# Performance work log

Measured on AMD Instinct MI355X. Metric: run time of the kernel, lower is better.

## Reference

```python
import jax, jax.numpy as jnp
import numpy as np

B, D, T, H, K = 16, 1024, 1024, 1024, 2  # batch, in_channels, seq_len, hidden_size, kernel_size


def setup_inputs() -> dict:
    key = jax.random.key(0)
    k1, k2, k3 = jax.random.split(key, 3)
    inputs = jax.random.normal(k1, (B, D, T), dtype=jnp.float32)
    # Conv1D kernel in OIH layout: [3H, D, K]; scaled to keep gates in a sane range
    conv_w = jax.random.normal(k2, (3 * H, D, K), dtype=jnp.float32) / np.float32(np.sqrt(D * K))
    conv_b = jax.random.normal(k3, (3 * H,), dtype=jnp.float32) * 0.01
    return {"inputs": inputs, "conv_w": conv_w, "conv_b": conv_b}


def reference(inputs, conv_w, conv_b):
    # inputs: [B, D, T] (channels_first, as in the keras call signature)
    # Causal conv: left-pad time by K-1, then VALID conv -> [B, 3H, T]
    padded = jnp.pad(inputs, ((0, 0), (0, 0), (K - 1, 0)))
    gates = jax.lax.conv_general_dilated(
        padded, conv_w, window_strides=(1,), padding="VALID",
        dimension_numbers=("NCH", "OIH", "NCH"))
    gates = gates + conv_b[None, :, None]
    gates = jnp.transpose(gates, (0, 2, 1))  # [B, T, 3H]
    z = jnp.tanh(gates[..., :H])
    f = jax.nn.sigmoid(gates[..., H:2 * H])
    o = jax.nn.sigmoid(gates[..., 2 * H:])

    # fo-pooling linear recurrence: c_t = f_t * c_{t-1} + (1 - f_t) * z_t, c_0 = 0
    zf = (jnp.transpose(z, (1, 0, 2)), jnp.transpose(f, (1, 0, 2)))  # time-major [T, B, H]

    def step(c, zf_t):
        z_t, f_t = zf_t
        c_new = f_t * c + (1.0 - f_t) * z_t
        return c_new, c_new

    c0 = jnp.zeros((B, H), dtype=inputs.dtype)
    _, c_seq = jax.lax.scan(step, c0, zf)
    c_seq = jnp.transpose(c_seq, (1, 0, 2))  # [B, T, H]
    h_seq = o * c_seq
    return c_seq, h_seq
```

## Files before the change

### kernel.cpp

```cpp
#include <hip/hip_runtime.h>

#define Bsz 16
#define Dch 1024
#define Tsz 1024
#define Hsz 1024
#define Mtot (Bsz*Tsz)
#define K2   (2*Dch)
#define Ntot (3*Hsz)
#define NCH  16
#define CL   64
#define NT   32

typedef __attribute__((ext_vector_type(8))) short bf16x8;
typedef __attribute__((ext_vector_type(4))) float f32x4;

__device__ __forceinline__ unsigned short f2bf(float x) {
    unsigned u = __float_as_uint(x);
    u += 0x7FFFu + ((u >> 16) & 1u);
    return (unsigned short)(u >> 16);
}
__device__ __forceinline__ float bf2f(unsigned short s) {
    return __uint_as_float(((unsigned)s) << 16);
}

#define GLOAD_LDS16(gp, lp) \
    __builtin_amdgcn_global_load_lds((const __attribute__((address_space(1))) void*)(gp), \
                                     (__attribute__((address_space(3))) void*)(lp), 16, 0, 0)

#define LDSB(p) ((unsigned)(unsigned long long)(__attribute__((address_space(3))) const void*)(p))

#define DSR(dst, addr, off) \
    asm volatile("ds_read_b128 %0, %1 offset:" #off : "=v"(dst) : "v"(addr))

__global__ __launch_bounds__(256)
void prep(const float* __restrict__ x, unsigned short* __restrict__ a2,
          const float* __restrict__ w, unsigned short* __restrict__ wb) {
    __shared__ float Xs[64][66];
    int bid = blockIdx.x;
    int tid = threadIdx.x;
    if (bid >= 4096) {
        int i0 = (bid - 4096) * 256 + tid;
        #pragma unroll
        for (int k = 0; k < 4; k++) {
            int i = i0 + k * (1536 * 256);
            float4 v = ((const float4*)w)[i];
            ushort4 r;
            r.x = f2bf(v.x); r.y = f2bf(v.y); r.z = f2bf(v.z); r.w = f2bf(v.w);
            ((ushort4*)wb)[i] = r;
        }
        return;
    }
    int b   = bid >> 8;
    int tt0 = ((bid >> 4) & 15) << 6;
    int dd0 = (bid & 15) << 6;
    int colt = tid & 63, rowq = tid >> 6;
    const size_t xbase = (size_t)b * (Dch * Tsz);
    #pragma unroll
    for (int r = 0; r < 16; r++) {
        int dd = r * 4 + rowq;
        Xs[dd][1 + colt] = x[xbase + (size_t)(dd0 + dd) * Tsz + tt0 + colt];
    }
    if (tid < 64) {
        Xs[tid][0] = (tt0 == 0) ? 0.f : x[xbase + (size_t)(dd0 + tid) * Tsz + tt0 - 1];
    }
    __syncthreads();
    #pragma unroll
    for (int r = 0; r < 16; r++) {
        int tr = r * 4 + rowq;
        int dc = colt;
        float v0 = Xs[dc][tr];
        float v1 = Xs[dc][tr + 1];
        unsigned pack = (unsigned)f2bf(v0) | ((unsigned)f2bf(v1) << 16);
        int m = (b << 10) + tt0 + tr;
        ((unsigned*)a2)[(size_t)m * (K2 / 2) + dd0 + dc] = pack;
    }
}

#define MFMA_PAIR(i0) do { \
    _Pragma("unroll") for (int ks_ = 0; ks_ < 2; ++ks_) { \
      _Pragma("unroll") for (int di_ = 0; di_ < 2; ++di_) { \
        _Pragma("unroll") for (int j_ = 0; j_ < 4; ++j_) { \
          acc[(i0)+di_][j_] = __builtin_amdgcn_mfma_f32_16x16x32_bf16( \
              af[(i0)+di_][ks_], bfr[ks_][j_], acc[(i0)+di_][j_], 0, 0, 0); \
        } } } } while (0)

__global__ __launch_bounds__(512, 2)
void gemm_gates(const unsigned short* __restrict__ A, const unsigned short* __restrict__ Bt,
                const float* __restrict__ bias,
                float* __restrict__ zc, float* __restrict__ fh, unsigned short* __restrict__ ob) {
    __shared__ __align__(16) unsigned short As[2][16384];
    __shared__ __align__(16) unsigned short Bs[2][16384];

    int tid  = threadIdx.x;
    int wv   = tid >> 6, lane = tid & 63;
    int wm   = wv >> 2, wn = wv & 3;
    int lm   = lane & 15, q = lane >> 4;

    int bid = blockIdx.x;
    int swz = (bid & 7) * 96 + (bid >> 3);
    int mt = swz / 12, nt = swz % 12;
    int m0 = mt << 8, n0 = nt << 8;

    const unsigned short* Abase = A  + (size_t)m0 * K2;
    const unsigned short* Bbase = Bt + (size_t)n0 * K2;

    int loff   = (wv * 8 + (lane >> 3)) * K2 + (((lane & 7) ^ (lane >> 3)) << 3);
    int ldsoff = wv * 8 * 64;

    int sw  = lm & 7;
    int kc0 = (q ^ sw) << 3;
    int kc1 = ((4 + q) ^ sw) << 3;
    int aoff = (wm * 128 + lm) * 64;
    int boff = (wn * 64 + lm) * 64;

    unsigned asb = LDSB(&As[0][0]);
    unsigned bsb = LDSB(&Bs[0][0]);
    unsigned aA0 = asb + (unsigned)(aoff + kc0) * 2u;
    unsigned aA1 = asb + (unsigned)(aoff + kc1) * 2u;
    unsigned aB0 = bsb + (unsigned)(boff + kc0) * 2u;
    unsigned aB1 = bsb + (unsigned)(boff + kc1) * 2u;

    f32x4 acc[8][4] = {};
    bf16x8 af[8][2], bfr[2][4];

#define STAGE_A(t, h) do { \
    const unsigned short* g_ = Abase + (h) * (128 * K2) + (t) * 64 + loff; \
    unsigned short* l_ = &As[(t) & 1][(h) * 8192 + ldsoff]; \
    GLOAD_LDS16(g_, l_); \
    GLOAD_LDS16(g_ + 64 * K2, l_ + 64 * 64); } while (0)
#define STAGE_B(t, h) do { \
    const unsigned short* g_ = Bbase + (h) * (128 * K2) + (t) * 64 + loff; \
    unsigned short* l_ = &Bs[(t) & 1][(h) * 8192 + ldsoff]; \
    GLOAD_LDS16(g_, l_); \
    GLOAD_LDS16(g_ + 64 * K2, l_ + 64 * 64); } while (0)

    STAGE_A(0, 0); STAGE_A(0, 1); STAGE_B(0, 0); STAGE_B(0, 1);
    STAGE_B(1, 1); STAGE_B(1, 0); STAGE_A(1, 0);
    asm volatile("s_waitcnt vmcnt(6)" ::: "memory");
    __builtin_amdgcn_s_barrier();

    #pragma unroll 2
    for (int t = 0; t < NT; ++t) {
        unsigned bufo = (t & 1) ? 32768u : 0u;
        unsigned tA0 = aA0 + bufo, tA1 = aA1 + bufo;
        unsigned tB0 = aB0 + bufo, tB1 = aB1 + bufo;

        DSR(bfr[0][0], tB0, 0);    DSR(bfr[0][1], tB0, 2048);
        DSR(bfr[0][2], tB0, 4096); DSR(bfr[0][3], tB0, 6144);
        DSR(bfr[1][0], tB1, 0);    DSR(bfr[1][1], tB1, 2048);
        DSR(bfr[1][2], tB1, 4096); DSR(bfr[1][3], tB1, 6144);
        DSR(af[0][0], tA0, 0);     DSR(af[0][1], tA1, 0);
        DSR(af[1][0], tA0, 2048);  DSR(af[1][1], tA1, 2048);
        if (t + 1 < NT) STAGE_A(t + 1, 1);
        asm volatile("s_waitcnt lgkmcnt(8)" ::: "memory");
        __builtin_amdgcn_sched_barrier(0);
        __builtin_amdgcn_s_barrier();
        asm volatile("s_waitcnt lgkmcnt(0)" ::: "memory");
        __builtin_amdgcn_sched_barrier(0);
        __builtin_amdgcn_s_setprio(1);
        MFMA_PAIR(0);
        __builtin_amdgcn_s_setprio(0);
        __builtin_amdgcn_sched_barrier(0);
        __builtin_amdgcn_s_barrier();

        DSR(af[2][0], tA0, 4096);  DSR(af[2][1], tA1, 4096);
        DSR(af[3][0], tA0, 6144);  DSR(af[3][1], tA1, 6144);
        if (t + 2 < NT) STAGE_B(t + 2, 1);
        __builtin_amdgcn_sched_barrier(0);
        __builtin_amdgcn_s_barrier();
        asm volatile("s_waitcnt lgkmcnt(0)" ::: "memory");
        __builtin_amdgcn_sched_barrier(0);
        __builtin_amdgcn_s_setprio(1);
        MFMA_PAIR(2);
        __builtin_amdgcn_s_setprio(0);
        __builtin_amdgcn_sched_barrier(0);
        __builtin_amdgcn_s_barrier();

        DSR(af[4][0], tA0, 8192);  DSR(af[4][1], tA1, 8192);
        DSR(af[5][0], tA0, 10240); DSR(af[5][1], tA1, 10240);
        DSR(af[6][0], tA0, 12288); DSR(af[6][1], tA1, 12288);
        DSR(af[7][0], tA0, 14336); DSR(af[7][1], tA1, 14336);
        if (t + 2 < NT) STAGE_B(t + 2, 0);
        __builtin_amdgcn_sched_barrier(0);
        __builtin_amdgcn_s_barrier();
        asm volatile("s_waitcnt lgkmcnt(0)" ::: "memory");
        __builtin_amdgcn_sched_barrier(0);
        __builtin_amdgcn_s_setprio(1);
        MFMA_PAIR(4);
        __builtin_amdgcn_s_setprio(0);
        __builtin_amdgcn_sched_barrier(0);
        __builtin_amdgcn_s_barrier();

        if (t + 2 < NT) STAGE_A(t + 2, 0);
        __builtin_amdgcn_sched_barrier(0);
        __builtin_amdgcn_s_barrier();
        __builtin_amdgcn_s_setprio(1);
        MFMA_PAIR(6);
        __builtin_amdgcn_s_setprio(0);
        __builtin_amdgcn_sched_barrier(0);
        if (t < NT - 2)       asm volatile("s_waitcnt vmcnt(6)" ::: "memory");
        else if (t == NT - 2) asm volatile("s_waitcnt vmcnt(0)" ::: "memory");
        __builtin_amdgcn_s_barrier();
    }

    int gt = nt >> 2;
    #pragma unroll
    for (int i = 0; i < 8; ++i) {
        int mrow = m0 + wm * 128 + i * 16 + q * 4;
        #pragma unroll
        for (int j = 0; j < 4; ++j) {
            int n = n0 + wn * 64 + j * 16 + lm;
            float bv = bias[n];
            int hcol = n & 1023;
            #pragma unroll
            for (int r = 0; r < 4; ++r) {
                float g = acc[i][j][r] + bv;
                size_t idx = (size_t)(mrow + r) * Hsz + hcol;
                if (gt == 0) {
                    float e = __expf(2.f * g);
                    zc[idx] = __fdividef(e - 1.f, e + 1.f);
                } else {
                    float s = __fdividef(1.f, 1.f + __expf(-g));
                    if (gt == 1) fh[idx] = s;
                    else         ob[idx] = f2bf(s);
                }
            }
        }
    }
}

__global__ __launch_bounds__(256)
void scan1(const float* __restrict__ zc, const float* __restrict__ fh,
           float* __restrict__ Aw, float* __restrict__ Bw) {
    int blk = blockIdx.x;
    int hb = blk & 1, ch = (blk >> 1) & 15, b = blk >> 5;
    int h = hb * 512 + threadIdx.x * 2;
    size_t base = ((size_t)b << 20) + ((size_t)(ch * CL) << 10) + h;
    float ax = 1.f, ay = 1.f, bx = 0.f, by = 0.f;
    #pragma unroll 8
    for (int s = 0; s < CL; s++) {
        size_t idx = base + ((size_t)s << 10);
        float2 z = *(const float2*)&zc[idx];
        float2 f = *(const float2*)&fh[idx];
        ax *= f.x; ay *= f.y;
        bx = z.x + f.x * (bx - z.x);
        by = z.y + f.y * (by - z.y);
    }
    int o = (ch * Bsz + b) * Hsz + h;
    *(float2*)&Aw[o] = make_float2(ax, ay);
    *(float2*)&Bw[o] = make_float2(bx, by);
}

__global__ __launch_bounds__(256)
void scan3(float* __restrict__ zc, float* __restrict__ fh,
           const unsigned short* __restrict__ ob,
           const float* __restrict__ Aw, const float* __restrict__ Bw) {
    int blk = blockIdx.x;
    int hb = blk & 1, ch = (blk >> 1) & 15, b = blk >> 5;
    int h = hb * 512 + threadIdx.x * 2;
    float cx = 0.f, cy = 0.f;
    for (int cp = 0; cp < ch; cp++) {
        int o = (cp * Bsz + b) * Hsz + h;
        float2 A = *(const float2*)&Aw[o];
        float2 B = *(const float2*)&Bw[o];
        cx = A.x * cx + B.x;
        cy = A.y * cy + B.y;
    }
    size_t base = ((size_t)b << 20) + ((size_t)(ch * CL) << 10) + h;
    #pragma unroll 8
    for (int s = 0; s < CL; s++) {
        size_t idx = base + ((size_t)s << 10);
        float2 z = *(const float2*)&zc[idx];
        float2 f = *(const float2*)&fh[idx];
        unsigned ov = *(const unsigned*)&ob[idx];
        cx = z.x + f.x * (cx - z.x);
        cy = z.y + f.y * (cy - z.y);
        *(float2*)&zc[idx] = make_float2(cx, cy);
        float ox = bf2f((unsigned short)(ov & 0xFFFF));
        float oy = bf2f((unsigned short)(ov >> 16));
        *(float2*)&fh[idx] = make_float2(ox * cx, oy * cy);
    }
}

extern "C" void kernel_launch(void* const* d_in, const int* in_sizes, int n_in,
                              void* d_out, int out_size, void* d_ws, size_t ws_size,
                              hipStream_t stream) {
    const float* x    = (const float*)d_in[0];
    const float* w    = (const float*)d_in[1];
    const float* bias = (const float*)d_in[2];
    float* zc = (float*)d_out;
    float* fh = (float*)d_out + (size_t)Mtot * Hsz;
    unsigned short* a2 = (unsigned short*)d_ws;
    unsigned short* wb = a2 + (size_t)Mtot * K2;
    unsigned short* ob = wb + (size_t)Ntot * K2;
    float* Aw = (float*)(ob + (size_t)Mtot * Hsz);
    float* Bw = Aw + NCH * Bsz * Hsz;

    hipLaunchKernelGGL(prep, dim3(5632), dim3(256), 0, stream, x, a2, w, wb);
    hipLaunchKernelGGL(gemm_gates, dim3(768), dim3(512), 0, stream, a2, wb, bias, zc, fh, ob);
    hipLaunchKernelGGL(scan1, dim3(512), dim3(256), 0, stream, zc, fh, Aw, Bw);
    hipLaunchKernelGGL(scan3, dim3(512), dim3(256), 0, stream, zc, fh, ob, Aw, Bw);
}
```

Measured before the change: 464.8 us.

## Reorder GEMM main loop into quadrant MFMA phases with cross-iteration LDS prefetch

Restructures the bf16 MFMA main loop so each iteration runs four 4x2 quadrant MFMA blocks instead of four 2x4 row pairs. The LDS fragment reads for the next k-tile (B cols 0-1, A rows 0-3) are issued at the end of the current iteration, and the final iteration is peeled. Partial lgkmcnt waits then let MFMAs start before all fragment reads land. The aim is to hide LDS read latency behind MFMA work and cut the number of barriers per k-step. The cost is a more delicate vmcnt/lgkmcnt accounting that is easy to get wrong, which risks races or stalls.

Measured after the change: 471.9 us. About the same (+1.5%).

```diff
diff --git a/kernel.cpp b/kernel.cpp
--- a/kernel.cpp
+++ b/kernel.cpp
@@ -31,6 +31,10 @@
 
 #define DSR(dst, addr, off) \
     asm volatile("ds_read_b128 %0, %1 offset:" #off : "=v"(dst) : "v"(addr))
+
+#define WAITLG(n) do { \
+    asm volatile("s_waitcnt lgkmcnt(" #n ")" ::: "memory"); \
+    __builtin_amdgcn_sched_barrier(0); } while (0)
 
 __global__ __launch_bounds__(256)
 void prep(const float* __restrict__ x, unsigned short* __restrict__ a2,
@@ -76,12 +80,12 @@
     }
 }
 
-#define MFMA_PAIR(i0) do { \
+#define MFMA_QUAD(a0, b0) do { \
     _Pragma("unroll") for (int ks_ = 0; ks_ < 2; ++ks_) { \
-      _Pragma("unroll") for (int di_ = 0; di_ < 2; ++di_) { \
-        _Pragma("unroll") for (int j_ = 0; j_ < 4; ++j_) { \
-          acc[(i0)+di_][j_] = __builtin_amdgcn_mfma_f32_16x16x32_bf16( \
-              af[(i0)+di_][ks_], bfr[ks_][j_], acc[(i0)+di_][j_], 0, 0, 0); \
+      _Pragma("unroll") for (int di_ = 0; di_ < 4; ++di_) { \
+        _Pragma("unroll") for (int dj_ = 0; dj_ < 2; ++dj_) { \
+          acc[(a0)*4+di_][(b0)*2+dj_] = __builtin_amdgcn_mfma_f32_16x16x32_bf16( \
+              af[(a0)*4+di_][ks_], bfr[ks_][(b0)*2+dj_], acc[(a0)*4+di_][(b0)*2+dj_], 0, 0, 0); \
         } } } } while (0)
 
 __global__ __launch_bounds__(512, 2)
@@ -134,73 +138,94 @@
     GLOAD_LDS16(g_, l_); \
     GLOAD_LDS16(g_ + 64 * K2, l_ + 64 * 64); } while (0)
 
+#define R_B01(bo) do { \
+    DSR(bfr[0][0], aB0 + (bo), 0);    DSR(bfr[1][0], aB1 + (bo), 0); \
+    DSR(bfr[0][1], aB0 + (bo), 2048); DSR(bfr[1][1], aB1 + (bo), 2048); } while (0)
+#define R_B23(bo) do { \
+    DSR(bfr[0][2], aB0 + (bo), 4096); DSR(bfr[1][2], aB1 + (bo), 4096); \
+    DSR(bfr[0][3], aB0 + (bo), 6144); DSR(bfr[1][3], aB1 + (bo), 6144); } while (0)
+#define R_A03(bo) do { \
+    DSR(af[0][0], aA0 + (bo), 0);    DSR(af[0][1], aA1 + (bo), 0); \
+    DSR(af[1][0], aA0 + (bo), 2048); DSR(af[1][1], aA1 + (bo), 2048); \
+    DSR(af[2][0], aA0 + (bo), 4096); DSR(af[2][1], aA1 + (bo), 4096); \
+    DSR(af[3][0], aA0 + (bo), 6144); DSR(af[3][1], aA1 + (bo), 6144); } while (0)
+#define R_A47(bo) do { \
+    DSR(af[4][0], aA0 + (bo), 8192);  DSR(af[4][1], aA1 + (bo), 8192); \
+    DSR(af[5][0], aA0 + (bo), 10240); DSR(af[5][1], aA1 + (bo), 10240); \
+    DSR(af[6][0], aA0 + (bo), 12288); DSR(af[6][1], aA1 + (bo), 12288); \
+    DSR(af[7][0], aA0 + (bo), 14336); DSR(af[7][1], aA1 + (bo), 14336); } while (0)
+
     STAGE_A(0, 0); STAGE_A(0, 1); STAGE_B(0, 0); STAGE_B(0, 1);
     STAGE_B(1, 1); STAGE_B(1, 0); STAGE_A(1, 0);
     asm volatile("s_waitcnt vmcnt(6)" ::: "memory");
     __builtin_amdgcn_s_barrier();
+    R_B01(0u); R_A03(0u);
+    __builtin_amdgcn_sched_barrier(0);
 
     #pragma unroll 2
-    for (int t = 0; t < NT; ++t) {
-        unsigned bufo = (t & 1) ? 32768u : 0u;
-        unsigned tA0 = aA0 + bufo, tA1 = aA1 + bufo;
-        unsigned tB0 = aB0 + bufo, tB1 = aB1 + bufo;
-
-        DSR(bfr[0][0], tB0, 0);    DSR(bfr[0][1], tB0, 2048);
-        DSR(bfr[0][2], tB0, 4096); DSR(bfr[0][3], tB0, 6144);
-        DSR(bfr[1][0], tB1, 0);    DSR(bfr[1][1], tB1, 2048);
-        DSR(bfr[1][2], tB1, 4096); DSR(bfr[1][3], tB1, 6144);
-        DSR(af[0][0], tA0, 0);     DSR(af[0][1], tA1, 0);
-        DSR(af[1][0], tA0, 2048);  DSR(af[1][1], tA1, 2048);
-        if (t + 1 < NT) STAGE_A(t + 1, 1);
-        asm volatile("s_waitcnt lgkmcnt(8)" ::: "memory");
-        __builtin_amdgcn_sched_barrier(0);
-        __builtin_amdgcn_s_barrier();
-        asm volatile("s_waitcnt lgkmcnt(0)" ::: "memory");
-        __builtin_amdgcn_sched_barrier(0);
-        __builtin_amdgcn_s_setprio(1);
-        MFMA_PAIR(0);
-        __builtin_amdgcn_s_setprio(0);
-        __builtin_amdgcn_sched_barrier(0);
-        __builtin_amdgcn_s_barrier();
-
-        DSR(af[2][0], tA0, 4096);  DSR(af[2][1], tA1, 4096);
-        DSR(af[3][0], tA0, 6144);  DSR(af[3][1], tA1, 6144);
+    for (int t = 0; t < NT - 1; ++t) {
+        unsigned cb = (t & 1) ? 32768u : 0u;
+        unsigned nb = cb ^ 32768u;
+
+        R_B23(cb);
+        STAGE_A(t + 1, 1);
+        WAITLG(4);
+        __builtin_amdgcn_s_setprio(1);
+        MFMA_QUAD(0, 0);
+        __builtin_amdgcn_s_setprio(0);
+        __builtin_amdgcn_sched_barrier(0);
+        __builtin_amdgcn_s_barrier();
+
+        R_A47(cb);
+        WAITLG(8);
+        __builtin_amdgcn_s_setprio(1);
+        MFMA_QUAD(0, 1);
+        __builtin_amdgcn_s_setprio(0);
+        __builtin_amdgcn_sched_barrier(0);
+        __builtin_amdgcn_s_barrier();
+
         if (t + 2 < NT) STAGE_B(t + 2, 1);
-        __builtin_amdgcn_sched_barrier(0);
-        __builtin_amdgcn_s_barrier();
-        asm volatile("s_waitcnt lgkmcnt(0)" ::: "memory");
-        __builtin_amdgcn_sched_barrier(0);
-        __builtin_amdgcn_s_setprio(1);
-        MFMA_PAIR(2);
-        __builtin_amdgcn_s_setprio(0);
-        __builtin_amdgcn_sched_barrier(0);
-        __builtin_amdgcn_s_barrier();
-
-        DSR(af[4][0], tA0, 8192);  DSR(af[4][1], tA1, 8192);
-        DSR(af[5][0], tA0, 10240); DSR(af[5][1], tA1, 10240);
-        DSR(af[6][0], tA0, 12288); DSR(af[6][1], tA1, 12288);
-        DSR(af[7][0], tA0, 14336); DSR(af[7][1], tA1, 14336);
-        if (t + 2 < NT) STAGE_B(t + 2, 0);
-        __builtin_amdgcn_sched_barrier(0);
-        __builtin_amdgcn_s_barrier();
-        asm volatile("s_waitcnt lgkmcnt(0)" ::: "memory");
-        __builtin_amdgcn_sched_barrier(0);
-        __builtin_amdgcn_s_setprio(1);
-        MFMA_PAIR(4);
-        __builtin_amdgcn_s_setprio(0);
-        __builtin_amdgcn_sched_barrier(0);
-        __builtin_amdgcn_s_barrier();
-
-        if (t + 2 < NT) STAGE_A(t + 2, 0);
-        __builtin_amdgcn_sched_barrier(0);
-        __builtin_amdgcn_s_barrier();
-        __builtin_amdgcn_s_setprio(1);
-        MFMA_PAIR(6);
-        __builtin_amdgcn_s_setprio(0);
-        __builtin_amdgcn_sched_barrier(0);
-        if (t < NT - 2)       asm volatile("s_waitcnt vmcnt(6)" ::: "memory");
-        else if (t == NT - 2) asm volatile("s_waitcnt vmcnt(0)" ::: "memory");
-        __builtin_amdgcn_s_barrier();
+        WAITLG(0);
+        __builtin_amdgcn_s_setprio(1);
+        MFMA_QUAD(1, 0);
+        __builtin_amdgcn_s_setprio(0);
+        __builtin_amdgcn_sched_barrier(0);
+        if (t + 2 < NT) asm volatile("s_waitcnt vmcnt(2)" ::: "memory");
+        else            asm volatile("s_waitcnt vmcnt(0)" ::: "memory");
+        __builtin_amdgcn_s_barrier();
+
+        R_B01(nb); R_A03(nb);
+        if (t + 2 < NT) { STAGE_B(t + 2, 0); STAGE_A(t + 2, 0); }
+        WAITLG(12);
+        __builtin_amdgcn_s_setprio(1);
+        MFMA_QUAD(1, 1);
+        __builtin_amdgcn_s_setprio(0);
+        __builtin_amdgcn_sched_barrier(0);
+        __builtin_amdgcn_s_barrier();
+    }
+
+    {
+        const unsigned cb = ((NT - 1) & 1) ? 32768u : 0u;
+        R_B23(cb);
+        WAITLG(4);
+        __builtin_amdgcn_s_setprio(1);
+        MFMA_QUAD(0, 0);
+        __builtin_amdgcn_s_setprio(0);
+        __builtin_amdgcn_sched_barrier(0);
+        __builtin_amdgcn_s_barrier();
+        R_A47(cb);
+        WAITLG(8);
+        __builtin_amdgcn_s_setprio(1);
+        MFMA_QUAD(0, 1);
+        __builtin_amdgcn_s_setprio(0);
+        __builtin_amdgcn_sched_barrier(0);
+        __builtin_amdgcn_s_barrier();
+        WAITLG(0);
+        __builtin_amdgcn_s_setprio(1);
+        MFMA_QUAD(1, 0);
+        MFMA_QUAD(1, 1);
+        __builtin_amdgcn_s_setprio(0);
+        __builtin_amdgcn_sched_barrier(0);
     }
 
     int gt = nt >> 2;
```

## Software-pipeline GEMM LDS fragment reads with double-buffered registers; split scan finer

Applied to the files above, without the earlier changes.

The GEMM main loop is rewritten as a manually unrolled two-iteration pipeline. A and B fragments are double-buffered in registers (afA/afB, bfrE/bfrO), so LDS reads for the next phase are issued before the current phase's MFMAs and fewer barriers and waitcnts sit on the critical path. B fragments for the next k-tile are prefetched during the current one, and an explicit tail handles the last iterations. Separately, the chunked scan uses 32 chunks of 32 steps instead of 16 of 64, doubling scan block count for more parallelism at the cost of a longer serial carry loop in scan3. The manual barrier and waitcnt schedule is intricate and risks races or extra register pressure.

Result: faster. 453.8 us (-2.4%).

```diff
diff --git a/kernel.cpp b/kernel.cpp
--- a/kernel.cpp
+++ b/kernel.cpp
@@ -7,8 +7,8 @@
 #define Mtot (Bsz*Tsz)
 #define K2   (2*Dch)
 #define Ntot (3*Hsz)
-#define NCH  16
-#define CL   64
+#define NCH  32
+#define CL   32
 #define NT   32
 
 typedef __attribute__((ext_vector_type(8))) short bf16x8;
@@ -31,6 +31,16 @@
 
 #define DSR(dst, addr, off) \
     asm volatile("ds_read_b128 %0, %1 offset:" #off : "=v"(dst) : "v"(addr))
+
+#define WAITLG(n) do { \
+    asm volatile("s_waitcnt lgkmcnt(" #n ")" ::: "memory"); \
+    __builtin_amdgcn_sched_barrier(0); } while (0)
+
+#define VMC(n) do { \
+    asm volatile("s_waitcnt vmcnt(" #n ")" ::: "memory"); \
+    __builtin_amdgcn_sched_barrier(0); } while (0)
+
+#define BAR __builtin_amdgcn_s_barrier()
 
 __global__ __launch_bounds__(256)
 void prep(const float* __restrict__ x, unsigned short* __restrict__ a2,
@@ -76,12 +86,12 @@
     }
 }
 
-#define MFMA_PAIR(i0) do { \
+#define MF(slot, bset, p) do { \
     _Pragma("unroll") for (int ks_ = 0; ks_ < 2; ++ks_) { \
-      _Pragma("unroll") for (int di_ = 0; di_ < 2; ++di_) { \
+      _Pragma("unroll") for (int d_ = 0; d_ < 2; ++d_) { \
         _Pragma("unroll") for (int j_ = 0; j_ < 4; ++j_) { \
-          acc[(i0)+di_][j_] = __builtin_amdgcn_mfma_f32_16x16x32_bf16( \
-              af[(i0)+di_][ks_], bfr[ks_][j_], acc[(i0)+di_][j_], 0, 0, 0); \
+          acc[2*(p)+d_][j_] = __builtin_amdgcn_mfma_f32_16x16x32_bf16( \
+              slot[d_][ks_], bset[ks_][j_], acc[2*(p)+d_][j_], 0, 0, 0); \
         } } } } while (0)
 
 __global__ __launch_bounds__(512, 2)
@@ -121,7 +131,8 @@
     unsigned aB1 = bsb + (unsigned)(boff + kc1) * 2u;
 
     f32x4 acc[8][4] = {};
-    bf16x8 af[8][2], bfr[2][4];
+    bf16x8 afA[2][2], afB[2][2];
+    bf16x8 bfrE[2][4], bfrO[2][4];
 
 #define STAGE_A(t, h) do { \
     const unsigned short* g_ = Abase + (h) * (128 * K2) + (t) * 64 + loff; \
@@ -134,74 +145,85 @@
     GLOAD_LDS16(g_, l_); \
     GLOAD_LDS16(g_ + 64 * K2, l_ + 64 * 64); } while (0)
 
+#define R_AFP(slot, o0, o1, bo) do { \
+    DSR(slot[0][0], aA0 + (bo), o0); DSR(slot[0][1], aA1 + (bo), o0); \
+    DSR(slot[1][0], aA0 + (bo), o1); DSR(slot[1][1], aA1 + (bo), o1); } while (0)
+#define R_BH0(set, bo) do { \
+    DSR(set[0][0], aB0 + (bo), 0);    DSR(set[1][0], aB1 + (bo), 0); \
+    DSR(set[0][1], aB0 + (bo), 2048); DSR(set[1][1], aB1 + (bo), 2048); } while (0)
+#define R_BH1(set, bo) do { \
+    DSR(set[0][2], aB0 + (bo), 4096); DSR(set[1][2], aB1 + (bo), 4096); \
+    DSR(set[0][3], aB0 + (bo), 6144); DSR(set[1][3], aB1 + (bo), 6144); } while (0)
+
+#define PRIO1 __builtin_amdgcn_s_setprio(1)
+#define PRIO0 do { __builtin_amdgcn_s_setprio(0); __builtin_amdgcn_sched_barrier(0); } while (0)
+
+#define PH0(T, CB, BC) do { \
+    R_AFP(afB, 4096, 6144, CB); \
+    STAGE_A((T) + 1, 1); \
+    WAITLG(4); \
+    PRIO1; MF(afA, BC, 0); PRIO0; } while (0)
+#define PH1(T, CB, NB, BC, BN) do { \
+    R_AFP(afA, 8192, 10240, CB); \
+    R_BH0(BN, NB); \
+    STAGE_A((T) + 1, 0); \
+    WAITLG(8); \
+    PRIO1; MF(afB, BC, 1); PRIO0; } while (0)
+#define PH2(T, CB, NB, BC, BN) do { \
+    R_AFP(afB, 12288, 14336, CB); \
+    R_BH1(BN, NB); \
+    STAGE_B((T) + 2, 1); \
+    WAITLG(8); \
+    PRIO1; MF(afA, BC, 2); PRIO0; } while (0)
+#define PH3(T, NB, BC) do { \
+    R_AFP(afA, 0, 2048, NB); \
+    STAGE_B((T) + 2, 0); \
+    WAITLG(4); \
+    PRIO1; MF(afB, BC, 3); PRIO0; } while (0)
+
     STAGE_A(0, 0); STAGE_A(0, 1); STAGE_B(0, 0); STAGE_B(0, 1);
-    STAGE_B(1, 1); STAGE_B(1, 0); STAGE_A(1, 0);
-    asm volatile("s_waitcnt vmcnt(6)" ::: "memory");
-    __builtin_amdgcn_s_barrier();
-
-    #pragma unroll 2
-    for (int t = 0; t < NT; ++t) {
-        unsigned bufo = (t & 1) ? 32768u : 0u;
-        unsigned tA0 = aA0 + bufo, tA1 = aA1 + bufo;
-        unsigned tB0 = aB0 + bufo, tB1 = aB1 + bufo;
-
-        DSR(bfr[0][0], tB0, 0);    DSR(bfr[0][1], tB0, 2048);
-        DSR(bfr[0][2], tB0, 4096); DSR(bfr[0][3], tB0, 6144);
-        DSR(bfr[1][0], tB1, 0);    DSR(bfr[1][1], tB1, 2048);
-        DSR(bfr[1][2], tB1, 4096); DSR(bfr[1][3], tB1, 6144);
-        DSR(af[0][0], tA0, 0);     DSR(af[0][1], tA1, 0);
-        DSR(af[1][0], tA0, 2048);  DSR(af[1][1], tA1, 2048);
-        if (t + 1 < NT) STAGE_A(t + 1, 1);
-        asm volatile("s_waitcnt lgkmcnt(8)" ::: "memory");
-        __builtin_amdgcn_sched_barrier(0);
-        __builtin_amdgcn_s_barrier();
-        asm volatile("s_waitcnt lgkmcnt(0)" ::: "memory");
-        __builtin_amdgcn_sched_barrier(0);
-        __builtin_amdgcn_s_setprio(1);
-        MFMA_PAIR(0);
-        __builtin_amdgcn_s_setprio(0);
-        __builtin_amdgcn_sched_barrier(0);
-        __builtin_amdgcn_s_barrier();
-
-        DSR(af[2][0], tA0, 4096);  DSR(af[2][1], tA1, 4096);
-        DSR(af[3][0], tA0, 6144);  DSR(af[3][1], tA1, 6144);
-        if (t + 2 < NT) STAGE_B(t + 2, 1);
-        __builtin_amdgcn_sched_barrier(0);
-        __builtin_amdgcn_s_barrier();
-        asm volatile("s_waitcnt lgkmcnt(0)" ::: "memory");
-        __builtin_amdgcn_sched_barrier(0);
-        __builtin_amdgcn_s_setprio(1);
-        MFMA_PAIR(2);
-        __builtin_amdgcn_s_setprio(0);
-        __builtin_amdgcn_sched_barrier(0);
-        __builtin_amdgcn_s_barrier();
-
-        DSR(af[4][0], tA0, 8192);  DSR(af[4][1], tA1, 8192);
-        DSR(af[5][0], tA0, 10240); DSR(af[5][1], tA1, 10240);
-        DSR(af[6][0], tA0, 12288); DSR(af[6][1], tA1, 12288);
-        DSR(af[7][0], tA0, 14336); DSR(af[7][1], tA1, 14336);
-        if (t + 2 < NT) STAGE_B(t + 2, 0);
-        __builtin_amdgcn_sched_barrier(0);
-        __builtin_amdgcn_s_barrier();
-        asm volatile("s_waitcnt lgkmcnt(0)" ::: "memory");
-        __builtin_amdgcn_sched_barrier(0);
-        __builtin_amdgcn_s_setprio(1);
-        MFMA_PAIR(4);
-        __builtin_amdgcn_s_setprio(0);
-        __builtin_amdgcn_sched_barrier(0);
-        __builtin_amdgcn_s_barrier();
-
-        if (t + 2 < NT) STAGE_A(t + 2, 0);
-        __builtin_amdgcn_sched_barrier(0);
-        __builtin_amdgcn_s_barrier();
-        __builtin_amdgcn_s_setprio(1);
-        MFMA_PAIR(6);
-        __builtin_amdgcn_s_setprio(0);
-        __builtin_amdgcn_sched_barrier(0);
-        if (t < NT - 2)       asm volatile("s_waitcnt vmcnt(6)" ::: "memory");
-        else if (t == NT - 2) asm volatile("s_waitcnt vmcnt(0)" ::: "memory");
-        __builtin_amdgcn_s_barrier();
-    }
+    STAGE_B(1, 1); STAGE_B(1, 0);
+    VMC(4); BAR;
+    R_AFP(afA, 0, 2048, 0u);
+    R_BH0(bfrE, 0u); R_BH1(bfrE, 0u);
+    __builtin_amdgcn_sched_barrier(0);
+
+    #pragma unroll 1
+    for (int tp = 0; tp < 15; ++tp) {
+        int t0 = 2 * tp;
+        PH0(t0, 0u, bfrE);                 VMC(2); BAR;
+        PH1(t0, 0u, 32768u, bfrE, bfrO);           BAR;
+        PH2(t0, 0u, 32768u, bfrE, bfrO);   VMC(2); BAR;
+        PH3(t0, 32768u, bfrE);                     BAR;
+        PH0(t0 + 1, 32768u, bfrO);         VMC(2); BAR;
+        PH1(t0 + 1, 32768u, 0u, bfrO, bfrE);       BAR;
+        PH2(t0 + 1, 32768u, 0u, bfrO, bfrE); VMC(2); BAR;
+        PH3(t0 + 1, 0u, bfrO);                     BAR;
+    }
+
+    PH0(30, 0u, bfrE);                     VMC(2); BAR;
+    PH1(30, 0u, 32768u, bfrE, bfrO);               BAR;
+    R_AFP(afB, 12288, 14336, 0u);
+    R_BH1(bfrO, 32768u);
+    WAITLG(8);
+    PRIO1; MF(afA, bfrE, 2); PRIO0;
+    VMC(0); BAR;
+    R_AFP(afA, 0, 2048, 32768u);
+    WAITLG(4);
+    PRIO1; MF(afB, bfrE, 3); PRIO0;
+    BAR;
+
+    R_AFP(afB, 4096, 6144, 32768u);
+    WAITLG(4);
+    PRIO1; MF(afA, bfrO, 0); PRIO0; BAR;
+    R_AFP(afA, 8192, 10240, 32768u);
+    WAITLG(4);
+    PRIO1; MF(afB, bfrO, 1); PRIO0; BAR;
+    R_AFP(afB, 12288, 14336, 32768u);
+    WAITLG(4);
+    PRIO1; MF(afA, bfrO, 2); PRIO0; BAR;
+    WAITLG(0);
+    PRIO1; MF(afB, bfrO, 3); PRIO0;
 
     int gt = nt >> 2;
     #pragma unroll
@@ -233,7 +255,7 @@
 void scan1(const float* __restrict__ zc, const float* __restrict__ fh,
            float* __restrict__ Aw, float* __restrict__ Bw) {
     int blk = blockIdx.x;
-    int hb = blk & 1, ch = (blk >> 1) & 15, b = blk >> 5;
+    int hb = blk & 1, ch = (blk >> 1) & 31, b = blk >> 6;
     int h = hb * 512 + threadIdx.x * 2;
     size_t base = ((size_t)b << 20) + ((size_t)(ch * CL) << 10) + h;
     float ax = 1.f, ay = 1.f, bx = 0.f, by = 0.f;
@@ -256,7 +278,7 @@
            const unsigned short* __restrict__ ob,
            const float* __restrict__ Aw, const float* __restrict__ Bw) {
     int blk = blockIdx.x;
-    int hb = blk & 1, ch = (blk >> 1) & 15, b = blk >> 5;
+    int hb = blk & 1, ch = (blk >> 1) & 31, b = blk >> 6;
     int h = hb * 512 + threadIdx.x * 2;
     float cx = 0.f, cy = 0.f;
     for (int cp = 0; cp < ch; cp++) {
@@ -298,6 +320,6 @@
 
     hipLaunchKernelGGL(prep, dim3(5632), dim3(256), 0, stream, x, a2, w, wb);
     hipLaunchKernelGGL(gemm_gates, dim3(768), dim3(512), 0, stream, a2, wb, bias, zc, fh, ob);
-    hipLaunchKernelGGL(scan1, dim3(512), dim3(256), 0, stream, zc, fh, Aw, Bw);
-    hipLaunchKernelGGL(scan3, dim3(512), dim3(256), 0, stream, zc, fh, ob, Aw, Bw);
-}
+    hipLaunchKernelGGL(scan1, dim3(1024), dim3(256), 0, stream, zc, fh, Aw, Bw);
+    hipLaunchKernelGGL(scan3, dim3(1024), dim3(256), 0, stream, zc, fh, ob, Aw, Bw);
+}
```
